# Optimization experiments

Hardware: AMD Instinct MI355X
Metric: run time of the kernel (lower is better)

Reference implementation:

```python
import jax, jax.numpy as jnp
import numpy as np

B, L, D, H = 2, 2048, 1024, 16
DH = D // H
SCALE = DH ** -0.5


def setup_inputs() -> dict:
    key = jax.random.key(0)
    k1, k2, k3 = jax.random.split(key, 3)
    x = jax.random.normal(k1, (B, L, D), dtype=jnp.float32)
    W_qkv = jax.random.normal(k2, (D, 3 * D), dtype=jnp.float32) * 0.02
    b_qkv = jnp.zeros((3 * D,), dtype=jnp.float32)
    W_proj = jax.random.normal(k3, (D, D), dtype=jnp.float32) * 0.02
    b_proj = jnp.zeros((D,), dtype=jnp.float32)
    return {"x": x, "W_qkv": W_qkv, "b_qkv": b_qkv, "W_proj": W_proj, "b_proj": b_proj}


def reference(x, W_qkv, b_qkv, W_proj, b_proj):
    b, l, d = x.shape
    # QKV projection: [B,L,3D] -> [3,B,H,L,DH] matching 'b n (three h d) -> three b h n d'
    qkv = (x @ W_qkv + b_qkv).reshape(b, l, 3, H, DH).transpose(2, 0, 3, 1, 4)
    q, k, v = qkv[0], qkv[1], qkv[2]
    # Causal scores. Chunking in the original is purely a scheduling detail;
    # masks are indexed by absolute row positions, so full attention is identical.
    scores = jnp.einsum('bhqd,bhkd->bhqk', q, k) * SCALE
    mask = jnp.triu(jnp.ones((l, l), dtype=bool), 1)  # True above diagonal
    neg_inf = jnp.finfo(scores.dtype).min
    scores = jnp.where(mask, neg_inf, scores)
    m = jnp.max(scores, axis=-1, keepdims=True)
    e = jnp.where(mask, 0.0, jnp.exp(scores - m))
    attn = e / (jnp.sum(e, axis=-1, keepdims=True) + 1e-6)
    out = jnp.einsum('bhqk,bhkd->bhqd', attn, v)  # [B,H,L,DH]
    out = out.transpose(0, 2, 1, 3).reshape(b, l, d)  # 'b h n d -> b n (h d)'
    return out @ W_proj + b_proj
```

## Files before the change

### kernel.cpp

```cpp
#include <hip/hip_runtime.h>


typedef __bf16 bf16x8 __attribute__((ext_vector_type(8)));
typedef float  f32x4  __attribute__((ext_vector_type(4)));
typedef unsigned short bhalf;
typedef unsigned int   uint32;

#define B_  2
#define L_  2048
#define D_  1024
#define H_  16
#define DH_ 64

#define GPTR(p) ((const __attribute__((address_space(1))) void*)(p))
#define SPTR(p) ((__attribute__((address_space(3))) void*)(p))

static __device__ __forceinline__ float bf2f(bhalf u) {
    union { uint32 u; float f; } x; x.u = ((uint32)u) << 16; return x.f;
}
static __device__ __forceinline__ bhalf f2bf(float f) {
    union { float f; uint32 u; } x; x.f = f;
    uint32 r = x.u + 0x7FFFu + ((x.u >> 16) & 1u);
    return (bhalf)(r >> 16);
}

__global__ void detect_dtype(const uint32* __restrict__ xw, int* __restrict__ flag) {
    int t = threadIdx.x;
    uint32 w = xw[t];
    uint32 e = (w >> 7) & 0xFFu;
    int g = (e < 0x6Fu || e > 0x84u) ? 1 : 0;
#pragma unroll
    for (int off = 32; off; off >>= 1) g += __shfl_xor(g, off);
    if (t == 0) *flag = (g > 16) ? 0 : 1;
}

__global__ void conv_bf16(const void* __restrict__ in, bhalf* __restrict__ out,
                          int n4, const int* __restrict__ flag) {
    const bool isb = (*flag != 0);
    for (int i = blockIdx.x * blockDim.x + threadIdx.x; i < n4;
         i += gridDim.x * blockDim.x) {
        if (isb) {
            ((uint2*)out)[i] = ((const uint2*)in)[i];
        } else {
            float4 v = ((const float4*)in)[i];
            uint2 o;
            o.x = (uint32)f2bf(v.x) | ((uint32)f2bf(v.y) << 16);
            o.y = (uint32)f2bf(v.z) | ((uint32)f2bf(v.w) << 16);
            ((uint2*)out)[i] = o;
        }
    }
}

__global__ void tr_conv(const void* __restrict__ in, bhalf* __restrict__ out,
                        int R, int C, const int* __restrict__ flag) {
    __shared__ bhalf t[32][33];
    const bool isb = (*flag != 0);
    int bx = blockIdx.x, by = blockIdx.y;
    int tx = threadIdx.x, ty = threadIdx.y;
#pragma unroll
    for (int i = 0; i < 32; i += 8) {
        size_t idx = (size_t)(by * 32 + ty + i) * C + bx * 32 + tx;
        t[ty + i][tx] = isb ? ((const bhalf*)in)[idx]
                            : f2bf(((const float*)in)[idx]);
    }
    __syncthreads();
#pragma unroll
    for (int i = 0; i < 32; i += 8)
        out[(size_t)(bx * 32 + ty + i) * R + by * 32 + tx] = t[tx][ty + i];
}


#define GSTAGE(BUF, KK) do {                                                  \
    int kko = (KK);                                                           \
    _Pragma("unroll")                                                         \
    for (int r = 0; r < 2; r++) {                                             \
        int c = r * 256 + tid;                                                \
        int row = c >> 2, p = c & 3;                                          \
        int gch = (p - row - (row >> 2)) & 3;                                 \
        __builtin_amdgcn_global_load_lds(                                     \
            GPTR(a0 + (size_t)row * K + kko + gch * 8),                       \
            SPTR(As[BUF] + (r * 256 + w * 64) * 8), 16, 0, 0);                \
        __builtin_amdgcn_global_load_lds(                                     \
            GPTR(b0 + (size_t)row * K + kko + gch * 8),                       \
            SPTR(Bs[BUF] + (r * 256 + w * 64) * 8), 16, 0, 0);                \
    }                                                                         \
} while (0)

template <int MODE>
__global__ __launch_bounds__(256) void gemm_bt(
        const bhalf* __restrict__ A, const bhalf* __restrict__ Bt,
        const void* __restrict__ bias,
        void* __restrict__ C0, bhalf* __restrict__ Qb,
        bhalf* __restrict__ Kb, bhalf* __restrict__ Vtb,
        int M, int N, int K, const int* __restrict__ flag) {
    __shared__ bhalf As[2][128 * 32];
    __shared__ bhalf Bs[2][128 * 32];
    const bool isb = (*flag != 0);
    const int tid  = threadIdx.x;
    const int w    = tid >> 6, lane = tid & 63;
    const int g    = lane >> 4, cl = lane & 15;
    const int m0   = blockIdx.y * 128, n0 = blockIdx.x * 128;
    const int wr   = (w >> 1) * 64, wc = (w & 1) * 64;

    f32x4 acc[4][4] = {};

    const bhalf* a0 = A  + (size_t)m0 * K;
    const bhalf* b0 = Bt + (size_t)n0 * K;

    GSTAGE(0, 0);
    __syncthreads();

    const int nk = K >> 5;
    for (int t = 0; t < nk; ++t) {
        int cur = t & 1;
        if (t + 1 < nk) GSTAGE(cur ^ 1, (t + 1) << 5);

        bf16x8 af[4], bf4[4];
#pragma unroll
        for (int i = 0; i < 4; i++) {
            int ra = wr + i * 16 + cl;
            af[i]  = *(const bf16x8*)(As[cur] + ra * 32 +
                                      (((g + ra + (ra >> 2)) & 3) * 8));
            int rb = wc + i * 16 + cl;
            bf4[i] = *(const bf16x8*)(Bs[cur] + rb * 32 +
                                      (((g + rb + (rb >> 2)) & 3) * 8));
        }
        __builtin_amdgcn_s_setprio(1);
#pragma unroll
        for (int i = 0; i < 4; i++)
#pragma unroll
            for (int j = 0; j < 4; j++)
                acc[i][j] = __builtin_amdgcn_mfma_f32_16x16x32_bf16(
                    af[i], bf4[j], acc[i][j], 0, 0, 0);
        __builtin_amdgcn_s_setprio(0);

        __syncthreads();
    }

#pragma unroll
    for (int i = 0; i < 4; i++) {
#pragma unroll
        for (int j = 0; j < 4; j++) {
            int nn = n0 + wc + j * 16 + cl;
            float bv = isb ? bf2f(((const bhalf*)bias)[nn])
                           : ((const float*)bias)[nn];
#pragma unroll
            for (int r = 0; r < 4; r++) {
                int mm = m0 + wr + i * 16 + g * 4 + r;
                float v = acc[i][j][r] + bv;
                if (MODE == 0) {
                    if (isb) ((bhalf*)C0)[(size_t)mm * N + nn] = f2bf(v);
                    else     ((float*)C0)[(size_t)mm * N + nn] = v;
                } else {
                    bhalf o = f2bf(v);
                    int b = mm >> 11, l = mm & 2047;
                    int three = nn >> 10, rem = nn & 1023;
                    int h = rem >> 6, dh = rem & 63;
                    size_t bh = (size_t)(b * 16 + h);
                    if (three == 0)      Qb [(bh * 2048 + l) * 64 + dh] = o;
                    else if (three == 1) Kb [(bh * 2048 + l) * 64 + dh] = o;
                    else                 Vtb[(bh * 64 + dh) * 2048 + l] = o;
                }
            }
        }
    }
}


#define STAGE(BUF, KT) do {                                                   \
    int ktv = (KT);                                                           \
    _Pragma("unroll")                                                         \
    for (int r = 0; r < 4; r++) {                                             \
        int c = r * 256 + tid;                                                \
        int row = c >> 3, p = c & 7;                                          \
        int fsw = (row & 3) | (((row >> 3) & 1) << 2);                        \
        __builtin_amdgcn_global_load_lds(                                     \
            GPTR(Kp + (size_t)(ktv * 128 + row) * 64 + (p ^ fsw) * 8),        \
            SPTR(Ks[BUF] + (r * 256 + w * 64) * 8), 16, 0, 0);                \
    }                                                                         \
    _Pragma("unroll")                                                         \
    for (int r = 0; r < 4; r++) {                                             \
        int c = r * 256 + tid;                                                \
        int row = c >> 4, p = c & 15;                                         \
        __builtin_amdgcn_global_load_lds(                                     \
            GPTR(Vt + (size_t)row * L_ + ktv * 128 + (p ^ (row & 15)) * 8),   \
            SPTR(Vs[BUF] + (r * 256 + w * 64) * 8), 16, 0, 0);                \
    }                                                                         \
} while (0)

#define ATTN_TILE(BUF, KT, QF, QLANE, MVAR, LVAR, OACC, MASK) do {            \
    f32x4 p8[8] = {};                                                         \
    _Pragma("unroll")                                                         \
    for (int s = 0; s < 2; s++) {                                             \
        bf16x8 kf[8];                                                         \
        _Pragma("unroll")                                                     \
        for (int j = 0; j < 8; j++) {                                         \
            int row = (j >> 1) * 32 + (cl >> 2) * 8 + (j & 1) * 4 + (cl & 3); \
            int fsw = (row & 3) | (((row >> 3) & 1) << 2);                    \
            int ch = s * 4 + g;                                               \
            kf[j] = *(const bf16x8*)(Ks[BUF] + row * 64 + ((ch ^ fsw) * 8));  \
        }                                                                     \
        __builtin_amdgcn_s_setprio(1);                                        \
        _Pragma("unroll")                                                     \
        for (int j = 0; j < 8; j++)                                           \
            p8[j] = __builtin_amdgcn_mfma_f32_16x16x32_bf16(                  \
                kf[j], QF[s], p8[j], 0, 0, 0);                                \
        __builtin_amdgcn_s_setprio(0);                                        \
    }                                                                         \
    float mx = -__builtin_inff();                                             \
    _Pragma("unroll")                                                         \
    for (int j = 0; j < 8; j++) {                                             \
        _Pragma("unroll")                                                     \
        for (int r = 0; r < 4; r++) {                                         \
            float v = p8[j][r] * 0.125f;                                      \
            if (MASK) {                                                       \
                int ka = (KT) * 128 + (j >> 1) * 32 + g * 8 + ((j & 1) << 2) + r; \
                v = (ka > (QLANE)) ? -__builtin_inff() : v;                   \
            }                                                                 \
            p8[j][r] = v;                                                     \
            mx = fmaxf(mx, v);                                                \
        }                                                                     \
    }                                                                         \
    mx = fmaxf(mx, __shfl_xor(mx, 16));                                       \
    mx = fmaxf(mx, __shfl_xor(mx, 32));                                       \
    float mnew = fmaxf(MVAR, mx);                                             \
    float alpha = __expf(MVAR - mnew);                                        \
    MVAR = mnew;                                                              \
    _Pragma("unroll")                                                         \
    for (int r = 0; r < 4; r++) {                                             \
        float ar = __shfl(alpha, g * 4 + r);                                  \
        _Pragma("unroll")                                                     \
        for (int dj = 0; dj < 4; dj++) OACC[dj][r] *= ar;                     \
    }                                                                         \
    float ls = 0.f;                                                           \
    _Pragma("unroll")                                                         \
    for (int j = 0; j < 8; j++)                                               \
        _Pragma("unroll")                                                     \
        for (int r = 0; r < 4; r++) {                                         \
            float e = __expf(p8[j][r] - mnew);                                \
            p8[j][r] = e;                                                     \
            ls += e;                                                          \
        }                                                                     \
    ls += __shfl_xor(ls, 16);                                                 \
    ls += __shfl_xor(ls, 32);                                                 \
    LVAR = LVAR * alpha + ls;                                                 \
    _Pragma("unroll")                                                         \
    for (int ks = 0; ks < 4; ks++) {                                          \
        bf16x8 pf;                                                            \
        _Pragma("unroll")                                                     \
        for (int e = 0; e < 8; e++)                                           \
            pf[e] = (__bf16)p8[2 * ks + (e >> 2)][e & 3];                     \
        bf16x8 vf[4];                                                         \
        _Pragma("unroll")                                                     \
        for (int dj = 0; dj < 4; dj++) {                                      \
            int vrow = dj * 16 + cl;                                          \
            int ch = ks * 4 + g;                                              \
            vf[dj] = *(const bf16x8*)(Vs[BUF] + vrow * 128 + ((ch ^ (vrow & 15)) * 8)); \
        }                                                                     \
        __builtin_amdgcn_s_setprio(1);                                        \
        _Pragma("unroll")                                                     \
        for (int dj = 0; dj < 4; dj++)                                        \
            OACC[dj] = __builtin_amdgcn_mfma_f32_16x16x32_bf16(               \
                pf, vf[dj], OACC[dj], 0, 0, 0);                               \
        __builtin_amdgcn_s_setprio(0);                                        \
    }                                                                         \
} while (0)

__global__ __launch_bounds__(256, 2) void attn_fwd(
        const bhalf* __restrict__ Qb, const bhalf* __restrict__ Kb,
        const bhalf* __restrict__ Vtb, bhalf* __restrict__ Ob) {
    __shared__ bhalf Ks[2][128 * 64];
    __shared__ bhalf Vs[2][64 * 128];

    const int bid  = blockIdx.x;
    const int xcd  = bid & 7, slot = bid >> 3;
    const int bx   = slot & 15;
    const int bh   = xcd + 8 * (slot >> 4);
    const int qbA  = 31 - bx;
    const int qbB  = bx;

    const int tid = threadIdx.x;
    const int w = tid >> 6, lane = tid & 63;
    const int g = lane >> 4, cl = lane & 15;

    const bhalf* Q  = Qb  + (size_t)bh * L_ * DH_;
    const bhalf* Kp = Kb  + (size_t)bh * L_ * DH_;
    const bhalf* Vt = Vtb + (size_t)bh * DH_ * L_;

    const int q0A = qbA * 64 + w * 16, qlA = q0A + cl;
    const int q0B = qbB * 64 + w * 16, qlB = q0B + cl;

    bf16x8 qfA[2], qfB[2];
#pragma unroll
    for (int s = 0; s < 2; s++) {
        qfA[s] = *(const bf16x8*)(Q + (size_t)(q0A + cl) * 64 + s * 32 + g * 8);
        qfB[s] = *(const bf16x8*)(Q + (size_t)(q0B + cl) * 64 + s * 32 + g * 8);
    }

    f32x4 oA[4] = {}, oB[4] = {};
    float mA = -__builtin_inff(), lA = 0.f;
    float mB = -__builtin_inff(), lB = 0.f;

    const int nktA = (qbA >> 1) + 1;
    const int nktB = (qbB >> 1) + 1;
    const int ntot = nktA + nktB;

    STAGE(0, 0);
    __syncthreads();

    for (int t = 0; t < ntot; ++t) {
        int cur = t & 1;
        if (t + 1 < ntot) {
            int tn = t + 1;
            int ktn = (tn < nktA) ? tn : (tn - nktA);
            STAGE(cur ^ 1, ktn);
        }
        if (t < nktA) {
            ATTN_TILE(cur, t, qfA, qlA, mA, lA, oA, (t == nktA - 1));
        } else {
            int kt = t - nktA;
            ATTN_TILE(cur, kt, qfB, qlB, mB, lB, oB, (kt == nktB - 1));
        }
        __syncthreads();
    }

    const int b = bh >> 4, h = bh & 15;
#pragma unroll
    for (int r = 0; r < 4; r++) {
        float lrA = __shfl(lA, g * 4 + r);
        float lrB = __shfl(lB, g * 4 + r);
        float invA = 1.f / (lrA + 1e-6f);
        float invB = 1.f / (lrB + 1e-6f);
        int qrA = q0A + g * 4 + r, qrB = q0B + g * 4 + r;
#pragma unroll
        for (int dj = 0; dj < 4; dj++) {
            Ob[((size_t)b * L_ + qrA) * D_ + h * 64 + dj * 16 + cl] =
                f2bf(oA[dj][r] * invA);
            Ob[((size_t)b * L_ + qrB) * D_ + h * 64 + dj * 16 + cl] =
                f2bf(oB[dj][r] * invB);
        }
    }
}

extern "C" void kernel_launch(void* const* d_in, const int* in_sizes, int n_in,
                              void* d_out, int out_size, void* d_ws, size_t ws_size,
                              hipStream_t stream) {
    const void* x     = d_in[0];
    const void* Wqkv  = d_in[1];
    const void* bqkv  = d_in[2];
    const void* Wproj = d_in[3];
    const void* bproj = d_in[4];

    char* ws = (char*)d_ws;
    const size_t SZ_FLG = 256;
    const size_t SZ_WQT = (size_t)3 * D_ * D_ * 2;
    const size_t SZ_WPT = (size_t)D_ * D_ * 2;
    const size_t SZ_X   = (size_t)B_ * L_ * D_ * 2;
    const size_t SZ_BUF = (size_t)B_ * H_ * L_ * DH_ * 2;

    int*   flag = (int*)ws;
    bhalf* Wq_t = (bhalf*)(ws + SZ_FLG);
    bhalf* Wp_t = (bhalf*)(ws + SZ_FLG + SZ_WQT);
    bhalf* Xb   = (bhalf*)(ws + SZ_FLG + SZ_WQT + SZ_WPT);
    bhalf* Qbuf = (bhalf*)(ws + SZ_FLG + SZ_WQT + SZ_WPT + SZ_X);
    bhalf* Kbuf = (bhalf*)(ws + SZ_FLG + SZ_WQT + SZ_WPT + SZ_X + SZ_BUF);
    bhalf* Vtbf = (bhalf*)(ws + SZ_FLG + SZ_WQT + SZ_WPT + SZ_X + 2 * SZ_BUF);
    bhalf* Obuf = (bhalf*)(ws + SZ_FLG + SZ_WQT + SZ_WPT + SZ_X + 3 * SZ_BUF);

    const int M = B_ * L_;

    detect_dtype<<<1, 64, 0, stream>>>((const uint32*)x, flag);

    conv_bf16<<<2048, 256, 0, stream>>>(x, Xb, (B_ * L_ * D_) / 4, flag);
    tr_conv<<<dim3(3 * D_ / 32, D_ / 32), dim3(32, 8), 0, stream>>>(
        Wqkv, Wq_t, D_, 3 * D_, flag);
    tr_conv<<<dim3(D_ / 32, D_ / 32), dim3(32, 8), 0, stream>>>(
        Wproj, Wp_t, D_, D_, flag);

    gemm_bt<1><<<dim3(3 * D_ / 128, M / 128), 256, 0, stream>>>(
        Xb, Wq_t, bqkv, nullptr, Qbuf, Kbuf, Vtbf, M, 3 * D_, D_, flag);

    attn_fwd<<<dim3(512), 256, 0, stream>>>(Qbuf, Kbuf, Vtbf, Obuf);

    gemm_bt<0><<<dim3(D_ / 128, M / 128), 256, 0, stream>>>(
        Obuf, Wp_t, bproj, d_out, nullptr, nullptr, nullptr, M, D_, D_, flag);
}
```

Before: 134.1 us.

## Fold softmax scale into Q, use exp2 with lazy rescale, share K/V tiles across query blocks

Q is pre-scaled by 0.125*log2(e) in the QKV epilogue, so the attention tile skips the per-score multiply and uses the native exp2 instruction. The running max is only updated, and the output and sum rescaled, when some lane's max grows by more than 8 in log2 units (skipped only when every lane qualifies). The max and sum reductions are split into four independent chains. The loop now streams each K/V tile once and applies it to both paired query blocks (B's tiles are a prefix of A's), roughly halving K/V loads and LDS staging. The risks are exponent growth up to 2^8 before rescaling, which is still safe in fp32, and that a stale max makes the bf16 P values less exact.

```diff
diff --git a/kernel.cpp b/kernel.cpp
--- a/kernel.cpp
+++ b/kernel.cpp
@@ -152,14 +152,17 @@
                     if (isb) ((bhalf*)C0)[(size_t)mm * N + nn] = f2bf(v);
                     else     ((float*)C0)[(size_t)mm * N + nn] = v;
                 } else {
-                    bhalf o = f2bf(v);
                     int b = mm >> 11, l = mm & 2047;
                     int three = nn >> 10, rem = nn & 1023;
                     int h = rem >> 6, dh = rem & 63;
                     size_t bh = (size_t)(b * 16 + h);
-                    if (three == 0)      Qb [(bh * 2048 + l) * 64 + dh] = o;
-                    else if (three == 1) Kb [(bh * 2048 + l) * 64 + dh] = o;
-                    else                 Vtb[(bh * 64 + dh) * 2048 + l] = o;
+                    if (three == 0) {
+                        Qb[(bh * 2048 + l) * 64 + dh] = f2bf(v * 0.18033688f);
+                    } else if (three == 1) {
+                        Kb [(bh * 2048 + l) * 64 + dh] = f2bf(v);
+                    } else {
+                        Vtb[(bh * 64 + dh) * 2048 + l] = f2bf(v);
+                    }
                 }
             }
         }
@@ -207,43 +210,51 @@
                 kf[j], QF[s], p8[j], 0, 0, 0);                                \
         __builtin_amdgcn_s_setprio(0);                                        \
     }                                                                         \
-    float mx = -__builtin_inff();                                             \
+    float mx0 = -__builtin_inff(), mx1 = -__builtin_inff();                   \
+    float mx2 = -__builtin_inff(), mx3 = -__builtin_inff();                   \
     _Pragma("unroll")                                                         \
     for (int j = 0; j < 8; j++) {                                             \
-        _Pragma("unroll")                                                     \
-        for (int r = 0; r < 4; r++) {                                         \
-            float v = p8[j][r] * 0.125f;                                      \
-            if (MASK) {                                                       \
-                int ka = (KT) * 128 + (j >> 1) * 32 + g * 8 + ((j & 1) << 2) + r; \
-                v = (ka > (QLANE)) ? -__builtin_inff() : v;                   \
-            }                                                                 \
-            p8[j][r] = v;                                                     \
-            mx = fmaxf(mx, v);                                                \
+        float v0 = p8[j][0], v1 = p8[j][1], v2 = p8[j][2], v3 = p8[j][3];     \
+        if (MASK) {                                                           \
+            int ka = (KT) * 128 + (j >> 1) * 32 + g * 8 + ((j & 1) << 2);     \
+            v0 = (ka + 0 > (QLANE)) ? -__builtin_inff() : v0;                 \
+            v1 = (ka + 1 > (QLANE)) ? -__builtin_inff() : v1;                 \
+            v2 = (ka + 2 > (QLANE)) ? -__builtin_inff() : v2;                 \
+            v3 = (ka + 3 > (QLANE)) ? -__builtin_inff() : v3;                 \
+            p8[j][0] = v0; p8[j][1] = v1; p8[j][2] = v2; p8[j][3] = v3;       \
         }                                                                     \
-    }                                                                         \
+        mx0 = fmaxf(mx0, v0); mx1 = fmaxf(mx1, v1);                           \
+        mx2 = fmaxf(mx2, v2); mx3 = fmaxf(mx3, v3);                           \
+    }                                                                         \
+    float mx = fmaxf(fmaxf(mx0, mx1), fmaxf(mx2, mx3));                       \
     mx = fmaxf(mx, __shfl_xor(mx, 16));                                       \
     mx = fmaxf(mx, __shfl_xor(mx, 32));                                       \
-    float mnew = fmaxf(MVAR, mx);                                             \
-    float alpha = __expf(MVAR - mnew);                                        \
-    MVAR = mnew;                                                              \
-    _Pragma("unroll")                                                         \
-    for (int r = 0; r < 4; r++) {                                             \
-        float ar = __shfl(alpha, g * 4 + r);                                  \
-        _Pragma("unroll")                                                     \
-        for (int dj = 0; dj < 4; dj++) OACC[dj][r] *= ar;                     \
-    }                                                                         \
-    float ls = 0.f;                                                           \
-    _Pragma("unroll")                                                         \
-    for (int j = 0; j < 8; j++)                                               \
+    if (!__all(mx - MVAR <= 8.f)) {       \
+        float mnew = fmaxf(MVAR, mx);                                         \
+        float alpha = __builtin_amdgcn_exp2f(MVAR - mnew);                    \
+        MVAR = mnew;                                                          \
+        LVAR *= alpha;                                                        \
         _Pragma("unroll")                                                     \
         for (int r = 0; r < 4; r++) {                                         \
-            float e = __expf(p8[j][r] - mnew);                                \
-            p8[j][r] = e;                                                     \
-            ls += e;                                                          \
+            float ar = __shfl(alpha, g * 4 + r);                              \
+            _Pragma("unroll")                                                 \
+            for (int dj = 0; dj < 4; dj++) OACC[dj][r] *= ar;                 \
         }                                                                     \
+    }                                                                         \
+    float s0 = 0.f, s1 = 0.f, s2 = 0.f, s3 = 0.f;                             \
+    _Pragma("unroll")                                                         \
+    for (int j = 0; j < 8; j++) {                                             \
+        float e0 = __builtin_amdgcn_exp2f(p8[j][0] - MVAR);                   \
+        float e1 = __builtin_amdgcn_exp2f(p8[j][1] - MVAR);                   \
+        float e2 = __builtin_amdgcn_exp2f(p8[j][2] - MVAR);                   \
+        float e3 = __builtin_amdgcn_exp2f(p8[j][3] - MVAR);                   \
+        p8[j][0] = e0; p8[j][1] = e1; p8[j][2] = e2; p8[j][3] = e3;           \
+        s0 += e0; s1 += e1; s2 += e2; s3 += e3;                               \
+    }                                                                         \
+    float ls = (s0 + s1) + (s2 + s3);                                         \
     ls += __shfl_xor(ls, 16);                                                 \
     ls += __shfl_xor(ls, 32);                                                 \
-    LVAR = LVAR * alpha + ls;                                                 \
+    LVAR += ls;                                                               \
     _Pragma("unroll")                                                         \
     for (int ks = 0; ks < 4; ks++) {                                          \
         bf16x8 pf;                                                            \
@@ -303,24 +314,17 @@
 
     const int nktA = (qbA >> 1) + 1;
     const int nktB = (qbB >> 1) + 1;
-    const int ntot = nktA + nktB;
 
     STAGE(0, 0);
     __syncthreads();
 
-    for (int t = 0; t < ntot; ++t) {
-        int cur = t & 1;
-        if (t + 1 < ntot) {
-            int tn = t + 1;
-            int ktn = (tn < nktA) ? tn : (tn - nktA);
-            STAGE(cur ^ 1, ktn);
-        }
-        if (t < nktA) {
-            ATTN_TILE(cur, t, qfA, qlA, mA, lA, oA, (t == nktA - 1));
-        } else {
-            int kt = t - nktA;
+    for (int kt = 0; kt < nktA; ++kt) {
+        int cur = kt & 1;
+        if (kt + 1 < nktA) STAGE(cur ^ 1, kt + 1);
+        if (kt < nktB) {
             ATTN_TILE(cur, kt, qfB, qlB, mB, lB, oB, (kt == nktB - 1));
         }
+        ATTN_TILE(cur, kt, qfA, qlA, mA, lA, oA, (kt == nktA - 1));
         __syncthreads();
     }
 
```

Result: faster. 125.0 us (-6.8%).
